# Kernel tuning notes

Measured on AMD Instinct MI355X. Metric: run time of the kernel, lower is better.

The kernel has to match this reference:

```python
import jax, jax.numpy as jnp
import numpy as np

N = 50000      # nodes
E = 500000     # edges
IN = 256       # input feature dim
HID = 64       # hidden (per-head) dim, layer 1
H1 = 4         # heads, layer 1
NC = 64        # num_classes (layer 2 out, 1 head)
ED = 32        # edge_dim
T = 8          # num_etypes
SLOPE = 0.2    # leakyrelu negative slope


def setup_inputs() -> dict:
    key = jax.random.key(0)
    ks = jax.random.split(key, 20)
    p = lambda k, shape: (jax.random.normal(k, shape, jnp.float32) * 0.05)
    return {
        "h": jax.random.normal(ks[0], (N, IN), jnp.float32),
        "row": jax.random.randint(ks[1], (E,), 0, N, jnp.int32),   # src
        "col": jax.random.randint(ks[2], (E,), 0, N, jnp.int32),   # dst
        "etype": jax.random.randint(ks[3], (E,), 0, T, jnp.int32),
        # layer 1 (4 heads, no residual, elu activation)
        "edge_emb1": p(ks[4], (T, ED)),
        "W1": p(ks[5], (IN, HID * H1)),
        "Wr1": p(ks[6], (T, ED, ED * H1)),      # TypedLinear per-etype weight
        "a_l1": p(ks[7], (H1, HID)),
        "a_r1": p(ks[8], (H1, HID)),
        "a_e1": p(ks[9], (H1, ED)),
        # layer 2 (1 head, residual Linear, no activation)
        "edge_emb2": p(ks[10], (T, ED)),
        "W2": p(ks[11], (HID * H1, NC)),
        "Wr2": p(ks[12], (T, ED, ED)),
        "a_l2": p(ks[13], (1, NC)),
        "a_r2": p(ks[14], (1, NC)),
        "a_e2": p(ks[15], (1, ED)),
        "res_W2": p(ks[16], (HID * H1, NC)),
        "res_b2": p(ks[17], (NC,)),
    }


def _simple_hgn_conv(h, row, col, etype, edge_emb, W, Wr, a_l, a_r, a_e,
                     res_W, res_b, apply_act):
    """One SimpleHGNConv layer. h:[N,in], returns [N, out_dim*H] (D-major, H-minor
    layout, matching emb.permute(0,2,1).view in the torch code)."""
    H, D = a_l.shape            # num_heads, out_dim
    n = h.shape[0]
    emb = (h @ W).reshape(n, H, D)                     # [N,H,D]
    emb = jnp.where(jnp.isnan(emb), 0.0, emb)
    # TypedLinear: edge_emb[etype] @ Wr[etype]; only T distinct rows -> per-type GEMM
    ee = jnp.einsum('te,teo->to', edge_emb, Wr).reshape(T, H, ED)  # [T,H,ED]
    h_l = jnp.einsum('nhd,hd->nh', emb, a_l)[row]      # [E,H]
    h_r = jnp.einsum('nhd,hd->nh', emb, a_r)[col]      # [E,H]
    h_e = jnp.einsum('thd,hd->th', ee, a_e)[etype]     # [E,H]
    att = jax.nn.leaky_relu(h_l + h_r + h_e, SLOPE)    # [E,H]
    # edge_softmax: normalize over incoming edges of each destination node (col)
    seg_max = jax.ops.segment_max(att, col, num_segments=n)   # [N,H]
    att = jnp.exp(att - seg_max[col])
    seg_sum = jax.ops.segment_sum(att, col, num_segments=n)   # [N,H]
    alpha = att / seg_sum[col]                          # [E,H]
    # u_mul_e + sum aggregation
    msg = emb[row] * alpha[:, :, None]                  # [E,H,D]
    out = jax.ops.segment_sum(msg, col, num_segments=n) # [N,H,D]
    out = out.transpose(0, 2, 1).reshape(n, D * H)      # D-major layout
    if res_W is not None:
        out = out + h @ res_W + res_b
    if apply_act:
        out = jax.nn.elu(out)
    return out


def reference(h, row, col, etype,
              edge_emb1, W1, Wr1, a_l1, a_r1, a_e1,
              edge_emb2, W2, Wr2, a_l2, a_r2, a_e2, res_W2, res_b2):
    h1 = _simple_hgn_conv(h, row, col, etype, edge_emb1, W1, Wr1,
                          a_l1, a_r1, a_e1, None, None, True)
    h2 = _simple_hgn_conv(h1, row, col, etype, edge_emb2, W2, Wr2,
                          a_l2, a_r2, a_e2, res_W2, res_b2, False)
    # split by node type (first half type 'l', second half type 'v')
    return (h2[: N // 2], h2[N // 2 :])
```

## Files before the change

kernel.cpp:

```cpp
#include <hip/hip_runtime.h>
#include <hip/hip_bf16.h>

typedef __bf16 bf16x8 __attribute__((ext_vector_type(8)));
typedef float f32x4 __attribute__((ext_vector_type(4)));

#define IN_DIM 256
#define NT 8

__device__ __forceinline__ float b2f(unsigned short u) {
  union { unsigned int i; float f; } x; x.i = ((unsigned int)u) << 16; return x.f;
}
__device__ __forceinline__ float lo2f(unsigned int w) {
  union { unsigned int i; float f; } x; x.i = w << 16; return x.f;
}
__device__ __forceinline__ float hi2f(unsigned int w) {
  union { unsigned int i; float f; } x; x.i = w & 0xFFFF0000u; return x.f;
}
__device__ __forceinline__ unsigned short f2b(float f) {
  union { float f; unsigned int i; } u; u.f = f;
  unsigned int r = u.i + 0x7FFF + ((u.i >> 16) & 1);
  return (unsigned short)(r >> 16);
}
__device__ __forceinline__ float lrelu(float x) { return x >= 0.f ? x : 0.2f * x; }
__device__ __forceinline__ float ldf(const void* p, size_t i, int isf32) {
  return isf32 ? ((const float*)p)[i] : b2f(((const unsigned short*)p)[i]);
}

__global__ void prep_all_kernel(const void* __restrict__ W1, const void* __restrict__ W2,
                                const void* __restrict__ rW2,
                                const void* __restrict__ al1, const void* __restrict__ ar1,
                                const void* __restrict__ al2, const void* __restrict__ ar2,
                                const void* __restrict__ ee1, const void* __restrict__ Wr1,
                                const void* __restrict__ ae1,
                                const void* __restrict__ ee2, const void* __restrict__ Wr2,
                                const void* __restrict__ ae2,
                                unsigned short* __restrict__ W1t,
                                unsigned short* __restrict__ W2t,
                                float* __restrict__ a2l, float* __restrict__ a2r,
                                float* __restrict__ he1, float* __restrict__ he2,
                                float* __restrict__ alD, float* __restrict__ arD,
                                const unsigned int* __restrict__ hw,
                                const int* __restrict__ col, int* __restrict__ cnt,
                                int E_, int N_, int* __restrict__ dflag) {
  int b = blockIdx.x, tid = threadIdx.x;
  if (b >= 454) {
    int base = (b - 454) * 1024 + tid;
#pragma unroll
    for (int k = 0; k < 4; k++) {
      int e = base + k * 256;
      if (e < E_) {
        int c = col[e];
        if ((unsigned)c < (unsigned)N_) atomicAdd(&cnt[c], 1);
      }
    }
    return;
  }
  __shared__ int sflag;
  {
    int bad = 0;
    if (tid < 64) {
      for (int i = 0; i < 4; i++) {
        unsigned int w = hw[tid * 4 + i];
        unsigned int ex = (w & 0x7FFFu) >> 7;
        if (ex >= 0xC0u) bad++;
      }
#pragma unroll
      for (int off = 32; off; off >>= 1) bad += __shfl_xor(bad, off);
      if (tid == 0) sflag = (bad > 8) ? 1 : 0;
    }
    __syncthreads();
  }
  const int isf32 = sflag;
  if (b == 0 && tid == 0) *dflag = isf32;
  if (b < 384) {
    int j = b, k = tid;
    if (j < 256) {
      int src = (j & 3) * 64 + (j >> 2);
      W1t[j * 256 + k] = f2b(ldf(W1, (size_t)k * 256 + src, isf32));
    } else {
      int o = j - 256;
      float v = (o < 64) ? ldf(W2, (size_t)k * 64 + o, isf32)
                         : ldf(rW2, (size_t)k * 64 + (o - 64), isf32);
      W2t[o * 256 + k] = f2b(v);
    }
  } else if (b < 448) {
    int k = (b - 384) * 4 + (tid >> 6), d = tid & 63;
    float w2 = ldf(W2, (size_t)k * 64 + d, isf32);
    float l2 = w2 * ldf(al2, d, isf32);
    float r2 = w2 * ldf(ar2, d, isf32);
#pragma unroll
    for (int off = 32; off; off >>= 1) { l2 += __shfl_xor(l2, off); r2 += __shfl_xor(r2, off); }
    if (d == 0) { a2l[k] = l2; a2r[k] = r2; }
  } else {
    int bid = b - 448;
    int t = tid >> 5, d = tid & 31;
    if (bid < 4) {
      int h = bid;
      float s = 0.f;
#pragma unroll
      for (int e = 0; e < 32; e++)
        s += ldf(ee1, t * 32 + e, isf32) * ldf(Wr1, (size_t)(t * 32 + e) * 128 + h * 32 + d, isf32);
      float v = s * ldf(ae1, h * 32 + d, isf32);
#pragma unroll
      for (int off = 16; off; off >>= 1) v += __shfl_xor(v, off);
      if (d == 0) he1[t * 4 + h] = v;
    } else if (bid == 4) {
      float s = 0.f;
#pragma unroll
      for (int e = 0; e < 32; e++)
        s += ldf(ee2, t * 32 + e, isf32) * ldf(Wr2, (size_t)(t * 32 + e) * 32 + d, isf32);
      float v = s * ldf(ae2, d, isf32);
#pragma unroll
      for (int off = 16; off; off >>= 1) v += __shfl_xor(v, off);
      if (d == 0) he2[t] = v;
    } else {
      int j = tid;
      alD[j] = ldf(al1, (j & 3) * 64 + (j >> 2), isf32);
      arD[j] = ldf(ar1, (j & 3) * 64 + (j >> 2), isf32);
    }
  }
}

__global__ __launch_bounds__(256, 2) void gemm1_fill(
    const void* __restrict__ A, int M,
    const unsigned short* __restrict__ Bt,
    unsigned short* __restrict__ emb1,
    const float* __restrict__ alD, const float* __restrict__ arD,
    float* __restrict__ hl1, float* __restrict__ hr1,
    const int* __restrict__ dflag, int MBlocks,
    const int* __restrict__ col, const int* __restrict__ row,
    const int* __restrict__ ety, const int* __restrict__ ptrb,
    const int* __restrict__ bsum, int* __restrict__ cnt,
    int* __restrict__ srcc, int E_) {
  __shared__ unsigned short As[64 * 64];
  __shared__ unsigned short Bs[256 * 64];
  __shared__ float lsum[4][64][4];
  __shared__ float rsum[4][64][4];
  if (blockIdx.x >= MBlocks) {
    int base = (blockIdx.x - MBlocks) * 1024 + threadIdx.x;
#pragma unroll
    for (int k = 0; k < 4; k++) {
      int e = base + k * 256;
      if (e < E_) {
        int c = col[e];
        if ((unsigned)c < (unsigned)M) {
          int pos = atomicSub(&cnt[c], 1) - 1;
          long long slot = (long long)(ptrb[c] + bsum[c >> 8]) + pos;
          if (slot >= 0 && slot < E_) {
            int sr = row[e], t = ety[e];
            srcc[slot] = ((unsigned)sr < (unsigned)M && (unsigned)t < (unsigned)NT)
                             ? (sr | (t << 20)) : -1;
          }
        }
      }
    }
    return;
  }
  int isf32 = *dflag;
  const int tid = threadIdx.x;
  const int m0 = blockIdx.x * 64;
  const int wv = tid >> 6, lane = tid & 63;
  const int q = lane >> 4, m = lane & 15;
  const int jp = wv * 64;
  f32x4 acc[4][4] = {};
  for (int kc = 0; kc < 256; kc += 64) {
    {
      int row_ = tid >> 2, qt = tid & 3;
      int gr = m0 + row_;
      unsigned short tmp[16];
      if (gr < M) {
        if (isf32) {
          const float* ap = (const float*)A + (size_t)gr * 256 + kc + qt * 16;
          float4 v0 = *(const float4*)ap;
          float4 v1 = *(const float4*)(ap + 4);
          float4 v2 = *(const float4*)(ap + 8);
          float4 v3 = *(const float4*)(ap + 12);
          tmp[0]=f2b(v0.x); tmp[1]=f2b(v0.y); tmp[2]=f2b(v0.z); tmp[3]=f2b(v0.w);
          tmp[4]=f2b(v1.x); tmp[5]=f2b(v1.y); tmp[6]=f2b(v1.z); tmp[7]=f2b(v1.w);
          tmp[8]=f2b(v2.x); tmp[9]=f2b(v2.y); tmp[10]=f2b(v2.z); tmp[11]=f2b(v2.w);
          tmp[12]=f2b(v3.x); tmp[13]=f2b(v3.y); tmp[14]=f2b(v3.z); tmp[15]=f2b(v3.w);
        } else {
          const unsigned short* ap = (const unsigned short*)A + (size_t)gr * 256 + kc + qt * 16;
          *(int4*)tmp = *(const int4*)ap;
          *(int4*)(tmp + 8) = *(const int4*)(ap + 8);
        }
      } else {
        for (int x = 0; x < 16; x++) tmp[x] = 0;
      }
      int g0 = (qt * 2) ^ (row_ & 7);
      int g1 = (qt * 2 + 1) ^ (row_ & 7);
      *(int4*)(As + row_ * 64 + g0 * 8) = *(int4*)tmp;
      *(int4*)(As + row_ * 64 + g1 * 8) = *(int4*)(tmp + 8);
    }
    {
#pragma unroll
      for (int i = 0; i < 8; i++) {
        int id = tid + i * 256;
        int row_ = id >> 3, gg = id & 7;
        int4 v = *(const int4*)(Bt + (size_t)row_ * 256 + kc + gg * 8);
        int pg = gg ^ (row_ & 7);
        *(int4*)(Bs + row_ * 64 + pg * 8) = v;
      }
    }
    __syncthreads();
#pragma unroll
    for (int ks = 0; ks < 2; ks++) {
      int gk = ks * 4 + q;
      bf16x8 afr[4];
#pragma unroll
      for (int cm = 0; cm < 4; cm++) {
        int row_ = cm * 16 + m;
        afr[cm] = *(const bf16x8*)(As + row_ * 64 + (gk ^ (row_ & 7)) * 8);
      }
#pragma unroll
      for (int cj = 0; cj < 4; cj++) {
        int jr = jp + cj * 16 + m;
        bf16x8 b = *(const bf16x8*)(Bs + jr * 64 + (gk ^ (jr & 7)) * 8);
#pragma unroll
        for (int cm = 0; cm < 4; cm++)
          acc[cm][cj] = __builtin_amdgcn_mfma_f32_16x16x32_bf16(afr[cm], b, acc[cm][cj], 0, 0, 0);
      }
    }
    __syncthreads();
  }
  float al[4], ar[4];
#pragma unroll
  for (int cj = 0; cj < 4; cj++) {
    al[cj] = alD[jp + cj * 16 + m];
    ar[cj] = arD[jp + cj * 16 + m];
  }
#pragma unroll
  for (int cm = 0; cm < 4; cm++) {
#pragma unroll
    for (int r = 0; r < 4; r++) {
      int lrow = cm * 16 + q * 4 + r;
      int gm = m0 + lrow;
      float lp = 0.f, rp = 0.f;
#pragma unroll
      for (int cj = 0; cj < 4; cj++) {
        float v = acc[cm][cj][r];
        if (gm < M) emb1[(size_t)gm * 256 + jp + cj * 16 + m] = f2b(v);
        lp += v * al[cj]; rp += v * ar[cj];
      }
      lp += __shfl_xor(lp, 4); lp += __shfl_xor(lp, 8);
      rp += __shfl_xor(rp, 4); rp += __shfl_xor(rp, 8);
      if (m < 4) { lsum[wv][lrow][m] = lp; rsum[wv][lrow][m] = rp; }
    }
  }
  __syncthreads();
  {
    int row_ = tid >> 2, h = tid & 3;
    int gm = m0 + row_;
    if (gm < M) {
      float l = lsum[0][row_][h] + lsum[1][row_][h] + lsum[2][row_][h] + lsum[3][row_][h];
      float r = rsum[0][row_][h] + rsum[1][row_][h] + rsum[2][row_][h] + rsum[3][row_][h];
      hl1[(size_t)gm * 4 + h] = l;
      hr1[(size_t)gm * 4 + h] = r;
    }
  }
}

__global__ __launch_bounds__(256, 2) void gemm2_fused(
    const unsigned short* __restrict__ A, int M,
    const unsigned short* __restrict__ Bt,
    unsigned short* __restrict__ emb2, unsigned short* __restrict__ res,
    const void* __restrict__ bias, const int* __restrict__ dflag) {
  __shared__ unsigned short As[64 * 64];
  __shared__ unsigned short Bs[128 * 64];
  int isf32 = *dflag;
  const int tid = threadIdx.x;
  const int m0 = blockIdx.x * 64;
  const int wv = tid >> 6, lane = tid & 63;
  const int q = lane >> 4, m = lane & 15;
  const int jp = (wv & 1) * 64;
  const int mh = (wv >> 1) * 32;
  f32x4 acc[2][4] = {};
  for (int kc = 0; kc < 256; kc += 64) {
    {
      int row = tid >> 2, qt = tid & 3;
      int gr = m0 + row;
      unsigned short tmp[16];
      if (gr < M) {
        const unsigned short* ap = A + (size_t)gr * 256 + kc + qt * 16;
        *(int4*)tmp = *(const int4*)ap;
        *(int4*)(tmp + 8) = *(const int4*)(ap + 8);
      } else {
        for (int x = 0; x < 16; x++) tmp[x] = 0;
      }
      int g0 = (qt * 2) ^ (row & 7);
      int g1 = (qt * 2 + 1) ^ (row & 7);
      *(int4*)(As + row * 64 + g0 * 8) = *(int4*)tmp;
      *(int4*)(As + row * 64 + g1 * 8) = *(int4*)(tmp + 8);
    }
    {
#pragma unroll
      for (int i = 0; i < 4; i++) {
        int id = tid + i * 256;
        int row = id >> 3, gg = id & 7;
        int4 v = *(const int4*)(Bt + (size_t)row * 256 + kc + gg * 8);
        int pg = gg ^ (row & 7);
        *(int4*)(Bs + row * 64 + pg * 8) = v;
      }
    }
    __syncthreads();
#pragma unroll
    for (int ks = 0; ks < 2; ks++) {
      int gk = ks * 4 + q;
      bf16x8 afr[2];
#pragma unroll
      for (int cm = 0; cm < 2; cm++) {
        int row = mh + cm * 16 + m;
        afr[cm] = *(const bf16x8*)(As + row * 64 + (gk ^ (row & 7)) * 8);
      }
#pragma unroll
      for (int cj = 0; cj < 4; cj++) {
        int jr = jp + cj * 16 + m;
        bf16x8 b = *(const bf16x8*)(Bs + jr * 64 + (gk ^ (jr & 7)) * 8);
#pragma unroll
        for (int cm = 0; cm < 2; cm++)
          acc[cm][cj] = __builtin_amdgcn_mfma_f32_16x16x32_bf16(afr[cm], b, acc[cm][cj], 0, 0, 0);
      }
    }
    __syncthreads();
  }
  float bv[4];
#pragma unroll
  for (int cj = 0; cj < 4; cj++)
    bv[cj] = (jp == 64) ? ldf(bias, cj * 16 + m, isf32) : 0.f;
#pragma unroll
  for (int cm = 0; cm < 2; cm++) {
#pragma unroll
    for (int r = 0; r < 4; r++) {
      int gm = m0 + mh + cm * 16 + q * 4 + r;
      if (gm < M) {
#pragma unroll
        for (int cj = 0; cj < 4; cj++) {
          float v = acc[cm][cj][r];
          int gj = cj * 16 + m;
          if (jp == 0) emb2[(size_t)gm * 64 + gj] = f2b(v);
          else res[(size_t)gm * 64 + gj] = f2b(v + bv[cj]);
        }
      }
    }
  }
}

__global__ void scan1_kernel(const int* __restrict__ cnt, int* __restrict__ ptrb,
                             int* __restrict__ bsum, int n) {
  __shared__ int wsum[4];
  int tid = threadIdx.x, lane = tid & 63, wid = tid >> 6;
  int i = blockIdx.x * 256 + tid;
  int v = (i < n) ? cnt[i] : 0;
  int x = v;
#pragma unroll
  for (int off = 1; off < 64; off <<= 1) {
    int y = __shfl_up(x, off);
    if (lane >= off) x += y;
  }
  if (lane == 63) wsum[wid] = x;
  __syncthreads();
  int woff = 0;
#pragma unroll
  for (int k = 0; k < 4; k++) woff += (k < wid) ? wsum[k] : 0;
  if (i < n) ptrb[i] = x - v + woff;
  if (tid == 255) bsum[blockIdx.x] = woff + x;
}

__global__ void scan2_kernel(int* __restrict__ bsum, int* __restrict__ ptrb,
                             int nb, int n) {
  __shared__ int wsum[4];
  int tid = threadIdx.x, lane = tid & 63, wid = tid >> 6;
  int v = (tid < nb) ? bsum[tid] : 0;
  int x = v;
#pragma unroll
  for (int off = 1; off < 64; off <<= 1) {
    int y = __shfl_up(x, off);
    if (lane >= off) x += y;
  }
  if (lane == 63) wsum[wid] = x;
  __syncthreads();
  int woff = 0;
#pragma unroll
  for (int k = 0; k < 4; k++) woff += (k < wid) ? wsum[k] : 0;
  if (tid < nb) bsum[tid] = x - v + woff;
  if (tid == 255) ptrb[n] = woff + x;
}

__global__ __launch_bounds__(256) void agg1_kernel(
    const int* __restrict__ ptrb, const int* __restrict__ bsumv,
    const int* __restrict__ srcc,
    const float* __restrict__ hl1, const float* __restrict__ hr1,
    const float* __restrict__ he1,
    const unsigned short* __restrict__ emb1, unsigned short* __restrict__ h1,
    const float* __restrict__ a2l, const float* __restrict__ a2r,
    float* __restrict__ hl2, float* __restrict__ hr2,
    int n0, int N_, int E_) {
  __shared__ float4 wds[4][64];
  __shared__ int sds[4][64];
  const int tid = threadIdx.x;
  const int wv = tid >> 6, lane = tid & 63;
  const int g = lane >> 4, ln = lane & 15;
  const int node = n0 + blockIdx.x * 16 + wv * 4 + g;
  const bool nv = node < N_;
  int p0 = 0, p1 = 0;
  if (nv) {
    p0 = ptrb[node] + bsumv[node >> 8];
    p1 = (node + 1 < N_) ? (ptrb[node + 1] + bsumv[(node + 1) >> 8]) : ptrb[N_];
    p0 = max(0, min(p0, E_)); p1 = max(p0, min(p1, E_));
  }
  float4 hrv = {0.f, 0.f, 0.f, 0.f};
  if (nv) hrv = *(const float4*)(hr1 + 4 * (size_t)node);
  float s0 = 0.f, s1 = 0.f, s2 = 0.f, s3 = 0.f;
  float acc[16];
#pragma unroll
  for (int k = 0; k < 16; k++) acc[k] = 0.f;
  const unsigned short* erow = emb1 + ln * 16;
  for (int pb = p0;; pb += 16) {
    if (!__any(pb < p1)) break;
    int mc = (pb < p1) ? min(p1 - pb, 16) : 0;
    float4 w = {0.f, 0.f, 0.f, 0.f};
    int src = 0;
    if (ln < mc) {
      int spk = srcc[pb + ln];
      if (spk >= 0) {
        int sr = spk & 0xFFFFF, t = spk >> 20;
        float4 a = *(const float4*)(hl1 + 4 * (size_t)sr);
        float4 ge = *(const float4*)(he1 + 4 * (size_t)t);
        w.x = __expf(lrelu(a.x + hrv.x + ge.x));
        w.y = __expf(lrelu(a.y + hrv.y + ge.y));
        w.z = __expf(lrelu(a.z + hrv.z + ge.z));
        w.w = __expf(lrelu(a.w + hrv.w + ge.w));
        src = sr;
      }
    }
    s0 += w.x; s1 += w.y; s2 += w.z; s3 += w.w;
    wds[wv][lane] = w;
    sds[wv][lane] = src;
    for (int j = 0; j < mc; j += 2) {
      bool v1 = (j + 1) < mc;
      float4 u0 = wds[wv][g * 16 + j];
      int r0 = sds[wv][g * 16 + j];
      const unsigned short* e0 = erow + (size_t)r0 * 256;
      int4 ra = *(const int4*)e0;
      int4 rb = *(const int4*)(e0 + 8);
      float4 u1; int4 rc, rd;
      if (v1) {
        u1 = wds[wv][g * 16 + j + 1];
        int r1 = sds[wv][g * 16 + j + 1];
        const unsigned short* e1 = erow + (size_t)r1 * 256;
        rc = *(const int4*)e1;
        rd = *(const int4*)(e1 + 8);
      }
      acc[0]  += u0.x * lo2f(ra.x); acc[1]  += u0.y * hi2f(ra.x);
      acc[2]  += u0.z * lo2f(ra.y); acc[3]  += u0.w * hi2f(ra.y);
      acc[4]  += u0.x * lo2f(ra.z); acc[5]  += u0.y * hi2f(ra.z);
      acc[6]  += u0.z * lo2f(ra.w); acc[7]  += u0.w * hi2f(ra.w);
      acc[8]  += u0.x * lo2f(rb.x); acc[9]  += u0.y * hi2f(rb.x);
      acc[10] += u0.z * lo2f(rb.y); acc[11] += u0.w * hi2f(rb.y);
      acc[12] += u0.x * lo2f(rb.z); acc[13] += u0.y * hi2f(rb.z);
      acc[14] += u0.z * lo2f(rb.w); acc[15] += u0.w * hi2f(rb.w);
      if (v1) {
        acc[0]  += u1.x * lo2f(rc.x); acc[1]  += u1.y * hi2f(rc.x);
        acc[2]  += u1.z * lo2f(rc.y); acc[3]  += u1.w * hi2f(rc.y);
        acc[4]  += u1.x * lo2f(rc.z); acc[5]  += u1.y * hi2f(rc.z);
        acc[6]  += u1.z * lo2f(rc.w); acc[7]  += u1.w * hi2f(rc.w);
        acc[8]  += u1.x * lo2f(rd.x); acc[9]  += u1.y * hi2f(rd.x);
        acc[10] += u1.z * lo2f(rd.y); acc[11] += u1.w * hi2f(rd.y);
        acc[12] += u1.x * lo2f(rd.z); acc[13] += u1.y * hi2f(rd.z);
        acc[14] += u1.z * lo2f(rd.w); acc[15] += u1.w * hi2f(rd.w);
      }
    }
  }
#pragma unroll
  for (int off = 1; off < 16; off <<= 1) {
    s0 += __shfl_xor(s0, off); s1 += __shfl_xor(s1, off);
    s2 += __shfl_xor(s2, off); s3 += __shfl_xor(s3, off);
  }
  float invs[4];
  invs[0] = s0 > 0.f ? 1.f / s0 : 0.f;
  invs[1] = s1 > 0.f ? 1.f / s1 : 0.f;
  invs[2] = s2 > 0.f ? 1.f / s2 : 0.f;
  invs[3] = s3 > 0.f ? 1.f / s3 : 0.f;
  float alv[16], arv[16];
#pragma unroll
  for (int q2 = 0; q2 < 4; q2++) {
    float4 t1 = *(const float4*)(a2l + ln * 16 + q2 * 4);
    float4 t2 = *(const float4*)(a2r + ln * 16 + q2 * 4);
    alv[q2 * 4 + 0] = t1.x; alv[q2 * 4 + 1] = t1.y;
    alv[q2 * 4 + 2] = t1.z; alv[q2 * 4 + 3] = t1.w;
    arv[q2 * 4 + 0] = t2.x; arv[q2 * 4 + 1] = t2.y;
    arv[q2 * 4 + 2] = t2.z; arv[q2 * 4 + 3] = t2.w;
  }
  float lp = 0.f, rp = 0.f;
  unsigned int ow[8];
#pragma unroll
  for (int k = 0; k < 16; k++) {
    float r = acc[k] * invs[k & 3];
    r = r > 0.f ? r : __expf(r) - 1.f;
    unsigned int bb = f2b(r);
    if ((k & 1) == 0) ow[k >> 1] = bb; else ow[k >> 1] |= bb << 16;
    lp += r * alv[k];
    rp += r * arv[k];
  }
  if (nv) {
    int4 va; va.x = ow[0]; va.y = ow[1]; va.z = ow[2]; va.w = ow[3];
    int4 vb; vb.x = ow[4]; vb.y = ow[5]; vb.z = ow[6]; vb.w = ow[7];
    *(int4*)(h1 + (size_t)node * 256 + ln * 16) = va;
    *(int4*)(h1 + (size_t)node * 256 + ln * 16 + 8) = vb;
  }
#pragma unroll
  for (int off = 1; off < 16; off <<= 1) {
    lp += __shfl_xor(lp, off); rp += __shfl_xor(rp, off);
  }
  if (nv && ln == 0) { hl2[node] = lp; hr2[node] = rp; }
}

__global__ __launch_bounds__(256) void agg2_kernel(
    const int* __restrict__ ptrb, const int* __restrict__ bsumv,
    const int* __restrict__ srcc,
    const float* __restrict__ hl2, const float* __restrict__ hr2,
    const float* __restrict__ he2,
    const unsigned short* __restrict__ emb2, const unsigned short* __restrict__ res,
    void* __restrict__ out, int N_, int E_, const int* __restrict__ dflag) {
  __shared__ int2 wsd[4][4][17];
  const int isf32 = *dflag;
  const int tid = threadIdx.x;
  const int wv = tid >> 6, lane = tid & 63;
  const int g = lane >> 4, ln = lane & 15;
  const int node = blockIdx.x * 16 + wv * 4 + g;
  const bool nv = node < N_;
  int p0 = 0, p1 = 0;
  if (nv) {
    p0 = ptrb[node] + bsumv[node >> 8];
    p1 = (node + 1 < N_) ? (ptrb[node + 1] + bsumv[(node + 1) >> 8]) : ptrb[N_];
    p0 = max(0, min(p0, E_)); p1 = max(p0, min(p1, E_));
  }
  float hrv = nv ? hr2[node] : 0.f;
  float s = 0.f;
  float acc[4] = {0.f, 0.f, 0.f, 0.f};
  const unsigned short* erow = emb2 + ln * 4;
  for (int pb = p0;; pb += 16) {
    if (!__any(pb < p1)) break;
    int mc = (pb < p1) ? min(p1 - pb, 16) : 0;
    float w = 0.f; int src = 0;
    if (ln < mc) {
      int spk = srcc[pb + ln];
      if (spk >= 0) {
        int sr = spk & 0xFFFFF, t = spk >> 20;
        w = __expf(lrelu(hl2[sr] + hrv + he2[t]));
        src = sr;
      }
    }
    s += w;
    int2 pk; pk.x = __float_as_int(w); pk.y = src;
    wsd[wv][g][ln] = pk;
    int2 w0 = {0, 0}, w1 = {0, 0}; int2 pa = {0, 0}, pc = {0, 0};
    if (0 < mc) { w0 = wsd[wv][g][0]; pa = *(const int2*)(erow + (size_t)w0.y * 64); }
    if (1 < mc) { w1 = wsd[wv][g][1]; pc = *(const int2*)(erow + (size_t)w1.y * 64); }
    for (int j = 0; j < mc; j += 2) {
      int2 nw0 = {0, 0}, nw1 = {0, 0}, na = {0, 0}, nc = {0, 0};
      if (j + 2 < mc) { nw0 = wsd[wv][g][j + 2]; na = *(const int2*)(erow + (size_t)nw0.y * 64); }
      if (j + 3 < mc) { nw1 = wsd[wv][g][j + 3]; nc = *(const int2*)(erow + (size_t)nw1.y * 64); }
      float u0 = __int_as_float(w0.x);
      acc[0] += u0 * lo2f(pa.x); acc[1] += u0 * hi2f(pa.x);
      acc[2] += u0 * lo2f(pa.y); acc[3] += u0 * hi2f(pa.y);
      if (j + 1 < mc) {
        float u1 = __int_as_float(w1.x);
        acc[0] += u1 * lo2f(pc.x); acc[1] += u1 * hi2f(pc.x);
        acc[2] += u1 * lo2f(pc.y); acc[3] += u1 * hi2f(pc.y);
      }
      w0 = nw0; w1 = nw1; pa = na; pc = nc;
    }
  }
#pragma unroll
  for (int off = 1; off < 16; off <<= 1) s += __shfl_xor(s, off);
  float inv = s > 0.f ? 1.f / s : 0.f;
  if (nv) {
    ushort4 rv = *(const ushort4*)(res + (size_t)node * 64 + ln * 4);
    float o0 = acc[0] * inv + b2f(rv.x);
    float o1 = acc[1] * inv + b2f(rv.y);
    float o2 = acc[2] * inv + b2f(rv.z);
    float o3 = acc[3] * inv + b2f(rv.w);
    size_t oi = (size_t)node * 64 + ln * 4;
    if (isf32) {
      float4 ov = {o0, o1, o2, o3};
      *(float4*)((float*)out + oi) = ov;
    } else {
      ushort4 ov; ov.x = f2b(o0); ov.y = f2b(o1); ov.z = f2b(o2); ov.w = f2b(o3);
      *(ushort4*)((unsigned short*)out + oi) = ov;
    }
  }
}

extern "C" void kernel_launch(void* const* d_in, const int* in_sizes, int n_in,
                              void* d_out, int out_size, void* d_ws, size_t ws_size,
                              hipStream_t stream) {
  const int N = in_sizes[0] / IN_DIM;
  const int E = in_sizes[1];

  const void* h   = d_in[0];
  const int* row  = (const int*)d_in[1];
  const int* col  = (const int*)d_in[2];
  const int* ety  = (const int*)d_in[3];
  const void* ee1 = d_in[4];
  const void* W1  = d_in[5];
  const void* Wr1 = d_in[6];
  const void* al1 = d_in[7];
  const void* ar1 = d_in[8];
  const void* ae1 = d_in[9];
  const void* ee2 = d_in[10];
  const void* W2  = d_in[11];
  const void* Wr2 = d_in[12];
  const void* al2 = d_in[13];
  const void* ar2 = d_in[14];
  const void* ae2 = d_in[15];
  const void* rW2 = d_in[16];
  const void* rb2 = d_in[17];

  char* p = (char*)d_ws;
  auto take = [&](size_t b) { char* q = p; p += (b + 255) & ~(size_t)255; return q; };
  unsigned short* h1   = (unsigned short*)take((size_t)N * 256 * 2);
  unsigned short* emb1 = (unsigned short*)take((size_t)N * 256 * 2);
  int* srcc = (int*)take((size_t)E * 4);
  int* ptrb = (int*)take((size_t)(N + 1) * 4);
  int* cnt  = (int*)take((size_t)N * 4);
  int* bsum = (int*)take(1024);
  float* hl1 = (float*)take((size_t)N * 4 * 4);
  float* hr1 = (float*)take((size_t)N * 4 * 4);
  float* hl2 = (float*)take((size_t)N * 4);
  float* hr2 = (float*)take((size_t)N * 4);
  unsigned short* W1t = (unsigned short*)take(256 * 256 * 2);
  unsigned short* W2t = (unsigned short*)take(128 * 256 * 2);
  float* a2l = (float*)take(256 * 4);
  float* a2r = (float*)take(256 * 4);
  float* alD = (float*)take(256 * 4);
  float* arD = (float*)take(256 * 4);
  float* he1 = (float*)take(NT * 4 * 4);
  float* he2 = (float*)take(NT * 4);
  int* dflag = (int*)take(256);
  unsigned short* emb2 = emb1;
  unsigned short* res  = emb1 + (size_t)N * 64;

  const size_t need = (size_t)(p - (char*)d_ws);
  if (need > ws_size) {
    hipMemsetAsync(d_out, 0, (size_t)out_size * 2, stream);
    return;
  }

  const int ECB = (E + 1023) / 1024;
  const int MB = (N + 63) / 64;
  const int SB = (N + 255) / 256;
  const int AB = (N + 15) / 16;

  hipMemsetAsync(cnt, 0, (size_t)N * 4, stream);
  prep_all_kernel<<<454 + ECB, 256, 0, stream>>>(
      W1, W2, rW2, al1, ar1, al2, ar2, ee1, Wr1, ae1, ee2, Wr2, ae2,
      W1t, W2t, a2l, a2r, he1, he2, alD, arD,
      (const unsigned int*)h, col, cnt, E, N, dflag);

  scan1_kernel<<<SB, 256, 0, stream>>>(cnt, ptrb, bsum, N);
  scan2_kernel<<<1, 256, 0, stream>>>(bsum, ptrb, SB, N);

  gemm1_fill<<<MB + ECB, 256, 0, stream>>>(
      h, N, W1t, emb1, alD, arD, hl1, hr1, dflag, MB,
      col, row, ety, ptrb, bsum, cnt, srcc, E);

  const int ABh = AB / 2;
  if (ABh > 0)
    agg1_kernel<<<ABh, 256, 0, stream>>>(
        ptrb, bsum, srcc, hl1, hr1, he1, emb1, h1, a2l, a2r, hl2, hr2, 0, N, E);
  agg1_kernel<<<AB - ABh, 256, 0, stream>>>(
      ptrb, bsum, srcc, hl1, hr1, he1, emb1, h1, a2l, a2r, hl2, hr2, ABh * 16, N, E);

  gemm2_fused<<<MB, 256, 0, stream>>>(h1, N, W2t, emb2, res, rb2, dflag);
  agg2_kernel<<<AB, 256, 0, stream>>>(
      ptrb, bsum, srcc, hl2, hr2, he2, emb2, res, d_out, N, E, dflag);
}
```

Baseline: 265.0 us.

## Shrink gemm1 tile, fuse scan passes, reorder fill blocks, merge agg1 launches

Cuts the gemm1 row tile from 64 to 32 and raises launch bounds to 4 blocks per SM for gemm1 and gemm2, aiming for more occupancy and better load balance. The CSR fill blocks now come first in the grid so scatter work starts early. The two-kernel scan becomes one kernel, where the last block to finish does the block-sum scan through an atomic counter. The split agg1 launch becomes a single launch. Smaller tiles reload B more often and the higher occupancy target may cause register spills.

Measured after the change: 256.8 us, median of 2. 3.1% less time.

```diff
diff --git a/kernel.cpp b/kernel.cpp
--- a/kernel.cpp
+++ b/kernel.cpp
@@ -20,6 +20,9 @@
   union { float f; unsigned int i; } u; u.f = f;
   unsigned int r = u.i + 0x7FFF + ((u.i >> 16) & 1);
   return (unsigned short)(r >> 16);
+}
+__device__ __forceinline__ unsigned int f2b2(float lo, float hi) {
+  return (unsigned int)f2b(lo) | ((unsigned int)f2b(hi) << 16);
 }
 __device__ __forceinline__ float lrelu(float x) { return x >= 0.f ? x : 0.2f * x; }
 __device__ __forceinline__ float ldf(const void* p, size_t i, int isf32) {
@@ -121,23 +124,23 @@
   }
 }
 
-__global__ __launch_bounds__(256, 2) void gemm1_fill(
+__global__ __launch_bounds__(256, 4) void gemm1_fill(
     const void* __restrict__ A, int M,
     const unsigned short* __restrict__ Bt,
     unsigned short* __restrict__ emb1,
     const float* __restrict__ alD, const float* __restrict__ arD,
     float* __restrict__ hl1, float* __restrict__ hr1,
-    const int* __restrict__ dflag, int MBlocks,
+    const int* __restrict__ dflag, int FillBlocks,
     const int* __restrict__ col, const int* __restrict__ row,
     const int* __restrict__ ety, const int* __restrict__ ptrb,
     const int* __restrict__ bsum, int* __restrict__ cnt,
     int* __restrict__ srcc, int E_) {
-  __shared__ unsigned short As[64 * 64];
+  __shared__ unsigned short As[32 * 64];
   __shared__ unsigned short Bs[256 * 64];
-  __shared__ float lsum[4][64][4];
-  __shared__ float rsum[4][64][4];
-  if (blockIdx.x >= MBlocks) {
-    int base = (blockIdx.x - MBlocks) * 1024 + threadIdx.x;
+  __shared__ float lsum[4][32][4];
+  __shared__ float rsum[4][32][4];
+  if (blockIdx.x < FillBlocks) {
+    int base = blockIdx.x * 1024 + threadIdx.x;
 #pragma unroll
     for (int k = 0; k < 4; k++) {
       int e = base + k * 256;
@@ -156,41 +159,34 @@
     }
     return;
   }
-  int isf32 = *dflag;
+  const int isf32 = *dflag;
   const int tid = threadIdx.x;
-  const int m0 = blockIdx.x * 64;
+  const int m0 = (blockIdx.x - FillBlocks) * 32;
   const int wv = tid >> 6, lane = tid & 63;
   const int q = lane >> 4, m = lane & 15;
   const int jp = wv * 64;
-  f32x4 acc[4][4] = {};
+  f32x4 acc[2][4] = {};
   for (int kc = 0; kc < 256; kc += 64) {
     {
-      int row_ = tid >> 2, qt = tid & 3;
+      int row_ = tid >> 3, qt = tid & 7;
       int gr = m0 + row_;
-      unsigned short tmp[16];
+      int4 w;
       if (gr < M) {
         if (isf32) {
-          const float* ap = (const float*)A + (size_t)gr * 256 + kc + qt * 16;
+          const float* ap = (const float*)A + (size_t)gr * 256 + kc + qt * 8;
           float4 v0 = *(const float4*)ap;
           float4 v1 = *(const float4*)(ap + 4);
-          float4 v2 = *(const float4*)(ap + 8);
-          float4 v3 = *(const float4*)(ap + 12);
-          tmp[0]=f2b(v0.x); tmp[1]=f2b(v0.y); tmp[2]=f2b(v0.z); tmp[3]=f2b(v0.w);
-          tmp[4]=f2b(v1.x); tmp[5]=f2b(v1.y); tmp[6]=f2b(v1.z); tmp[7]=f2b(v1.w);
-          tmp[8]=f2b(v2.x); tmp[9]=f2b(v2.y); tmp[10]=f2b(v2.z); tmp[11]=f2b(v2.w);
-          tmp[12]=f2b(v3.x); tmp[13]=f2b(v3.y); tmp[14]=f2b(v3.z); tmp[15]=f2b(v3.w);
+          w.x = (int)f2b2(v0.x, v0.y); w.y = (int)f2b2(v0.z, v0.w);
+          w.z = (int)f2b2(v1.x, v1.y); w.w = (int)f2b2(v1.z, v1.w);
         } else {
-          const unsigned short* ap = (const unsigned short*)A + (size_t)gr * 256 + kc + qt * 16;
-          *(int4*)tmp = *(const int4*)ap;
-          *(int4*)(tmp + 8) = *(const int4*)(ap + 8);
+          const unsigned short* ap = (const unsigned short*)A + (size_t)gr * 256 + kc + qt * 8;
+          w = *(const int4*)ap;
         }
       } else {
-        for (int x = 0; x < 16; x++) tmp[x] = 0;
-      }
-      int g0 = (qt * 2) ^ (row_ & 7);
-      int g1 = (qt * 2 + 1) ^ (row_ & 7);
-      *(int4*)(As + row_ * 64 + g0 * 8) = *(int4*)tmp;
-      *(int4*)(As + row_ * 64 + g1 * 8) = *(int4*)(tmp + 8);
+        w.x = 0; w.y = 0; w.z = 0; w.w = 0;
+      }
+      int pg = qt ^ (row_ & 7);
+      *(int4*)(As + row_ * 64 + pg * 8) = w;
     }
     {
 #pragma unroll
@@ -206,9 +202,9 @@
 #pragma unroll
     for (int ks = 0; ks < 2; ks++) {
       int gk = ks * 4 + q;
-      bf16x8 afr[4];
-#pragma unroll
-      for (int cm = 0; cm < 4; cm++) {
+      bf16x8 afr[2];
+#pragma unroll
+      for (int cm = 0; cm < 2; cm++) {
         int row_ = cm * 16 + m;
         afr[cm] = *(const bf16x8*)(As + row_ * 64 + (gk ^ (row_ & 7)) * 8);
       }
@@ -217,7 +213,7 @@
         int jr = jp + cj * 16 + m;
         bf16x8 b = *(const bf16x8*)(Bs + jr * 64 + (gk ^ (jr & 7)) * 8);
 #pragma unroll
-        for (int cm = 0; cm < 4; cm++)
+        for (int cm = 0; cm < 2; cm++)
           acc[cm][cj] = __builtin_amdgcn_mfma_f32_16x16x32_bf16(afr[cm], b, acc[cm][cj], 0, 0, 0);
       }
     }
@@ -230,7 +226,7 @@
     ar[cj] = arD[jp + cj * 16 + m];
   }
 #pragma unroll
-  for (int cm = 0; cm < 4; cm++) {
+  for (int cm = 0; cm < 2; cm++) {
 #pragma unroll
     for (int r = 0; r < 4; r++) {
       int lrow = cm * 16 + q * 4 + r;
@@ -248,7 +244,7 @@
     }
   }
   __syncthreads();
-  {
+  if (tid < 128) {
     int row_ = tid >> 2, h = tid & 3;
     int gm = m0 + row_;
     if (gm < M) {
@@ -260,7 +256,7 @@
   }
 }
 
-__global__ __launch_bounds__(256, 2) void gemm2_fused(
+__global__ __launch_bounds__(256, 4) void gemm2_fused(
     const unsigned short* __restrict__ A, int M,
     const unsigned short* __restrict__ Bt,
     unsigned short* __restrict__ emb2, unsigned short* __restrict__ res,
@@ -346,9 +342,12 @@
 }
 
 __global__ void scan1_kernel(const int* __restrict__ cnt, int* __restrict__ ptrb,
-                             int* __restrict__ bsum, int n) {
+                             int* __restrict__ bsum, int* __restrict__ done,
+                             int n, int nb) {
   __shared__ int wsum[4];
+  __shared__ int lastflag;
   int tid = threadIdx.x, lane = tid & 63, wid = tid >> 6;
+  if (tid == 0) lastflag = 0;
   int i = blockIdx.x * 256 + tid;
   int v = (i < n) ? cnt[i] : 0;
   int x = v;
@@ -364,26 +363,29 @@
   for (int k = 0; k < 4; k++) woff += (k < wid) ? wsum[k] : 0;
   if (i < n) ptrb[i] = x - v + woff;
   if (tid == 255) bsum[blockIdx.x] = woff + x;
-}
-
-__global__ void scan2_kernel(int* __restrict__ bsum, int* __restrict__ ptrb,
-                             int nb, int n) {
-  __shared__ int wsum[4];
-  int tid = threadIdx.x, lane = tid & 63, wid = tid >> 6;
-  int v = (tid < nb) ? bsum[tid] : 0;
-  int x = v;
-#pragma unroll
-  for (int off = 1; off < 64; off <<= 1) {
-    int y = __shfl_up(x, off);
-    if (lane >= off) x += y;
-  }
-  if (lane == 63) wsum[wid] = x;
   __syncthreads();
-  int woff = 0;
-#pragma unroll
-  for (int k = 0; k < 4; k++) woff += (k < wid) ? wsum[k] : 0;
-  if (tid < nb) bsum[tid] = x - v + woff;
-  if (tid == 255) ptrb[n] = woff + x;
+  if (tid == 255) {
+    __threadfence();
+    int t = atomicAdd(done, 1);
+    if (t == (int)gridDim.x - 1) { __threadfence(); lastflag = 1; }
+  }
+  __syncthreads();
+  if (lastflag) {
+    int v2 = (tid < nb) ? ((volatile int*)bsum)[tid] : 0;
+    int x2 = v2;
+#pragma unroll
+    for (int off = 1; off < 64; off <<= 1) {
+      int y = __shfl_up(x2, off);
+      if (lane >= off) x2 += y;
+    }
+    if (lane == 63) wsum[wid] = x2;
+    __syncthreads();
+    int woff2 = 0;
+#pragma unroll
+    for (int k = 0; k < 4; k++) woff2 += (k < wid) ? wsum[k] : 0;
+    if (tid < nb) bsum[tid] = x2 - v2 + woff2;
+    if (tid == 255) ptrb[n] = woff2 + x2;
+  }
 }
 
 __global__ __launch_bounds__(256) void agg1_kernel(
@@ -623,7 +625,7 @@
   unsigned short* emb1 = (unsigned short*)take((size_t)N * 256 * 2);
   int* srcc = (int*)take((size_t)E * 4);
   int* ptrb = (int*)take((size_t)(N + 1) * 4);
-  int* cnt  = (int*)take((size_t)N * 4);
+  int* cnt  = (int*)take((size_t)(N + 64) * 4);
   int* bsum = (int*)take(1024);
   float* hl1 = (float*)take((size_t)N * 4 * 4);
   float* hr1 = (float*)take((size_t)N * 4 * 4);
@@ -640,6 +642,7 @@
   int* dflag = (int*)take(256);
   unsigned short* emb2 = emb1;
   unsigned short* res  = emb1 + (size_t)N * 64;
+  int* done = cnt + N;
 
   const size_t need = (size_t)(p - (char*)d_ws);
   if (need > ws_size) {
@@ -648,29 +651,25 @@
   }
 
   const int ECB = (E + 1023) / 1024;
+  const int MB32 = (N + 31) / 32;
   const int MB = (N + 63) / 64;
   const int SB = (N + 255) / 256;
   const int AB = (N + 15) / 16;
 
-  hipMemsetAsync(cnt, 0, (size_t)N * 4, stream);
+  hipMemsetAsync(cnt, 0, (size_t)(N + 64) * 4, stream);
   prep_all_kernel<<<454 + ECB, 256, 0, stream>>>(
       W1, W2, rW2, al1, ar1, al2, ar2, ee1, Wr1, ae1, ee2, Wr2, ae2,
       W1t, W2t, a2l, a2r, he1, he2, alD, arD,
       (const unsigned int*)h, col, cnt, E, N, dflag);
 
-  scan1_kernel<<<SB, 256, 0, stream>>>(cnt, ptrb, bsum, N);
-  scan2_kernel<<<1, 256, 0, stream>>>(bsum, ptrb, SB, N);
-
-  gemm1_fill<<<MB + ECB, 256, 0, stream>>>(
-      h, N, W1t, emb1, alD, arD, hl1, hr1, dflag, MB,
+  scan1_kernel<<<SB, 256, 0, stream>>>(cnt, ptrb, bsum, done, N, SB);
+
+  gemm1_fill<<<ECB + MB32, 256, 0, stream>>>(
+      h, N, W1t, emb1, alD, arD, hl1, hr1, dflag, ECB,
       col, row, ety, ptrb, bsum, cnt, srcc, E);
 
-  const int ABh = AB / 2;
-  if (ABh > 0)
-    agg1_kernel<<<ABh, 256, 0, stream>>>(
-        ptrb, bsum, srcc, hl1, hr1, he1, emb1, h1, a2l, a2r, hl2, hr2, 0, N, E);
-  agg1_kernel<<<AB - ABh, 256, 0, stream>>>(
-      ptrb, bsum, srcc, hl1, hr1, he1, emb1, h1, a2l, a2r, hl2, hr2, ABh * 16, N, E);
+  agg1_kernel<<<AB, 256, 0, stream>>>(
+      ptrb, bsum, srcc, hl1, hr1, he1, emb1, h1, a2l, a2r, hl2, hr2, 0, N, E);
 
   gemm2_fused<<<MB, 256, 0, stream>>>(h1, N, W2t, emb2, res, rb2, dflag);
   agg2_kernel<<<AB, 256, 0, stream>>>(
```
